# Kernel optimization log

Measured on AMD Instinct MI355X. Metric: run time of the kernel, lower is better.

The kernel has to match this reference:

```python
import math
import jax, jax.numpy as jnp
import numpy as np

N_LAYERS = 6
N_HEADS = 8
WINDOW = 4
LN_EPS = 1e-6


def _get_rel_emb(emb, length):
    # emb: [1, 2*WINDOW+1, kc] -> [1, 2*length-1, kc]
    max_rel = 2 * WINDOW + 1
    pad = max(0, length - (WINDOW + 1))
    start = max(0, WINDOW + 1 - length)
    end = max_rel + 2 * length - 1
    if pad > 0:
        emb = jnp.pad(emb, ((0, 0), (pad, pad), (0, 0)))
    return emb[:, start:end]


def _rel_to_abs(x):
    # x: [b,h,l,2l-1] -> [b,h,l,l]
    b, h, l, _ = x.shape
    x = jnp.pad(x, ((0, 0), (0, 0), (0, 0), (0, 1)))
    xf = x.reshape(b, h, l * 2 * l)
    xf = jnp.pad(xf, ((0, 0), (0, 0), (0, l - 1)))
    return xf.reshape(b, h, l + 1, 2 * l - 1)[:, :, :l, l - 1:]


def _abs_to_rel(x):
    # x: [b,h,l,l] -> [b,h,l,2l-1]
    b, h, l, _ = x.shape
    x = jnp.pad(x, ((0, 0), (0, 0), (0, 0), (0, l - 1)))
    xf = x.reshape(b, h, -1)
    xf = jnp.pad(xf, ((0, 0), (0, 0), (l, 0)))
    return xf.reshape(b, h, l, 2 * l)[..., 1:]


def _layer_norm(x, scale, bias):
    m = jnp.mean(x, axis=-1, keepdims=True)
    v = jnp.mean(jnp.square(x - m), axis=-1, keepdims=True)
    return (x - m) * jax.lax.rsqrt(v + LN_EPS) * scale + bias


def _forward(x, x_mask, Wq, bq, Wk, bk, Wv, bv, Wo, bo, emb_rel_k, emb_rel_v,
             ln1_scale, ln1_bias, W1, b1, W2, b2, ln2_scale, ln2_bias):
    B, T, C = x.shape
    H = N_HEADS
    KC = C // H
    scale = 1.0 / math.sqrt(KC)
    attn_mask = x_mask[:, :, None, :] * x_mask[:, :, :, None]  # [B,1,T,T]
    mask_t = jnp.transpose(x_mask, (0, 2, 1))  # [B,T,1]
    x = x * mask_t
    for l in range(N_LAYERS):
        # --- relative-position multi-head self-attention ---
        q = (x @ Wq[l] + bq[l]).reshape(B, T, H, KC).transpose(0, 2, 1, 3)
        k = (x @ Wk[l] + bk[l]).reshape(B, T, H, KC).transpose(0, 2, 1, 3)
        v = (x @ Wv[l] + bv[l]).reshape(B, T, H, KC).transpose(0, 2, 1, 3)
        scores = jnp.einsum('bhqd,bhkd->bhqk', q * scale, k)
        rk = _get_rel_emb(emb_rel_k[l], T)[0]  # [2T-1, KC] (heads shared)
        rel_logits = jnp.einsum('bhld,md->bhlm', q * scale, rk)
        scores = scores + _rel_to_abs(rel_logits)
        scores = jnp.where(attn_mask == 0, -10000.0, scores)
        p = jax.nn.softmax(scores, axis=-1)
        out = jnp.einsum('bhqk,bhkd->bhqd', p, v)
        rv = _get_rel_emb(emb_rel_v[l], T)[0]
        out = out + jnp.einsum('bhlm,md->bhld', _abs_to_rel(p), rv)
        out = out.transpose(0, 2, 1, 3).reshape(B, T, C)
        y = out @ Wo[l] + bo[l]
        x = _layer_norm(x + y, ln1_scale[l], ln1_bias[l])
        # --- pointwise conv FFN (kernel_size=1) ---
        h1 = jax.nn.relu((x * mask_t) @ W1[l] + b1[l])
        y = (h1 * mask_t) @ W2[l] + b2[l]
        y = y * mask_t
        x = _layer_norm(x + y, ln2_scale[l], ln2_bias[l])
    return x * mask_t


def setup_inputs() -> dict:
    key = jax.random.key(0)
    B, T, C, F, L, H = 8, 768, 512, 2048, N_LAYERS, N_HEADS
    KC = C // H
    ks = jax.random.split(key, 10)
    nrm = lambda k, s, sd=0.02: jax.random.normal(k, s, jnp.float32) * sd
    return {
        'x': jax.random.normal(ks[0], (B, T, C), jnp.float32),
        'x_mask': jnp.ones((B, 1, T), jnp.float32),
        'Wq': nrm(ks[1], (L, C, C)), 'bq': jnp.zeros((L, C), jnp.float32),
        'Wk': nrm(ks[2], (L, C, C)), 'bk': jnp.zeros((L, C), jnp.float32),
        'Wv': nrm(ks[3], (L, C, C)), 'bv': jnp.zeros((L, C), jnp.float32),
        'Wo': nrm(ks[4], (L, C, C)), 'bo': jnp.zeros((L, C), jnp.float32),
        'emb_rel_k': nrm(ks[5], (L, 1, 2 * WINDOW + 1, KC), KC ** -0.5),
        'emb_rel_v': nrm(ks[6], (L, 1, 2 * WINDOW + 1, KC), KC ** -0.5),
        'ln1_scale': jnp.ones((L, C), jnp.float32), 'ln1_bias': jnp.zeros((L, C), jnp.float32),
        'W1': nrm(ks[7], (L, C, F)), 'b1': jnp.zeros((L, F), jnp.float32),
        'W2': nrm(ks[8], (L, F, C)), 'b2': jnp.zeros((L, C), jnp.float32),
        'ln2_scale': jnp.ones((L, C), jnp.float32), 'ln2_bias': jnp.zeros((L, C), jnp.float32),
    }


def reference(x, x_mask, Wq, bq, Wk, bk, Wv, bv, Wo, bo, emb_rel_k, emb_rel_v,
              ln1_scale, ln1_bias, W1, b1, W2, b2, ln2_scale, ln2_bias):
    return _forward(x, x_mask, Wq, bq, Wk, bk, Wv, bv, Wo, bo, emb_rel_k, emb_rel_v,
                    ln1_scale, ln1_bias, W1, b1, W2, b2, ln2_scale, ln2_bias)
```

## Files before the change

### kernel.cpp

```cpp
#include <hip/hip_runtime.h>
#include <stdint.h>


typedef unsigned short u16;
typedef __attribute__((ext_vector_type(8))) __bf16 bf16x8;
typedef __attribute__((ext_vector_type(4))) float f32x4;

#define B_ 8
#define T_ 768
#define C_ 512
#define F_ 2048
#define LOG2E 1.4426950408889634f

__device__ __forceinline__ float b2f(u16 u) {
    union { float f; uint32_t i; } x; x.i = ((uint32_t)u) << 16; return x.f;
}
__device__ __forceinline__ u16 f2b(float f) {
    union { float f; uint32_t i; } x; x.f = f;
    return (u16)((x.i + 0x7fffu + ((x.i >> 16) & 1u)) >> 16);
}

template <int EPI>
__global__ __launch_bounds__(256) void gemm_bt4(
    const u16* __restrict__ A, int aStride,
    const u16* __restrict__ Bt, int bStride,
    const float* __restrict__ bias,
    u16* __restrict__ out, int oStride, int K, float epiScale)
{
    const int tid = threadIdx.x;
    const int wave = tid >> 6, lane = tid & 63;
    const int wm = wave & 1, wn = wave >> 1;
    const int quad = lane >> 4, l16 = lane & 15;
    const int m0 = blockIdx.x * 64;
    const int n0 = blockIdx.y * 64;

    __shared__ u16 As[64 * 64];
    __shared__ u16 Bs[64 * 64];

    const f32x4 vzero = {0.f, 0.f, 0.f, 0.f};
    f32x4 acc[2][2];
#pragma unroll
    for (int i = 0; i < 2; ++i)
#pragma unroll
        for (int j = 0; j < 2; ++j) acc[i][j] = vzero;

    for (int k0 = 0; k0 < K; k0 += 64) {
#pragma unroll
        for (int i = 0; i < 2; ++i) {
            int c = tid + i * 256;
            int row = c >> 3, pc = c & 7, lc = pc ^ (row & 7);
            *(uint4*)&As[c * 8] =
                *(const uint4*)(A + (long long)(m0 + row) * aStride + (k0 + lc * 8));
            *(uint4*)&Bs[c * 8] =
                *(const uint4*)(Bt + (long long)(n0 + row) * bStride + (k0 + lc * 8));
        }
        __syncthreads();
        __builtin_amdgcn_s_setprio(1);
#pragma unroll
        for (int ks = 0; ks < 2; ++ks) {
            bf16x8 af[2], bfr[2];
#pragma unroll
            for (int mi = 0; mi < 2; ++mi) {
                int row = wm * 32 + mi * 16 + l16;
                int pc = ((ks << 2) | quad) ^ (row & 7);
                af[mi] = *(const bf16x8*)&As[row * 64 + pc * 8];
            }
#pragma unroll
            for (int ni = 0; ni < 2; ++ni) {
                int row = wn * 32 + ni * 16 + l16;
                int pc = ((ks << 2) | quad) ^ (row & 7);
                bfr[ni] = *(const bf16x8*)&Bs[row * 64 + pc * 8];
            }
#pragma unroll
            for (int mi = 0; mi < 2; ++mi)
#pragma unroll
                for (int ni = 0; ni < 2; ++ni)
                    acc[mi][ni] = __builtin_amdgcn_mfma_f32_16x16x32_bf16(
                        bfr[ni], af[mi], acc[mi][ni], 0, 0, 0);
        }
        __builtin_amdgcn_s_setprio(0);
        __syncthreads();
    }

#pragma unroll
    for (int mi = 0; mi < 2; ++mi) {
        int row = m0 + wm * 32 + mi * 16 + l16;
#pragma unroll
        for (int ni = 0; ni < 2; ++ni) {
            int colb = n0 + wn * 32 + ni * 16 + quad * 4;
            u16 pk[4];
#pragma unroll
            for (int r = 0; r < 4; ++r) {
                float v = acc[mi][ni][r] + bias[colb + r];
                if (EPI == 1) v = v > 0.f ? v : 0.f;
                if (EPI == 3) { if (colb + r < 512) v *= epiScale; }
                pk[r] = f2b(v);
            }
            uint2 p;
            p.x = (uint32_t)pk[0] | ((uint32_t)pk[1] << 16);
            p.y = (uint32_t)pk[2] | ((uint32_t)pk[3] << 16);
            *(uint2*)(out + (long long)row * oStride + colb) = p;
        }
    }
}

__global__ __launch_bounds__(256) void bandg_k(
    const u16* __restrict__ qkv, const float* __restrict__ erk,
    float* __restrict__ bandg)
{
    __shared__ float erkS[576];
    const int tid = threadIdx.x;
    for (int idx = tid; idx < 576; idx += 256) erkS[idx] = erk[idx];
    __syncthreads();
    const int gid = blockIdx.x * 256 + tid;
    const int row = gid >> 3, h = gid & 7;
    const u16* q = qkv + (long long)row * 1536 + h * 64;
    float acc[9];
#pragma unroll
    for (int e = 0; e < 9; ++e) acc[e] = 0.f;
#pragma unroll
    for (int c = 0; c < 8; ++c) {
        uint4 d4 = *(const uint4*)(q + c * 8);
        const uint32_t dw[4] = {d4.x, d4.y, d4.z, d4.w};
#pragma unroll
        for (int j = 0; j < 8; ++j) {
            u16 uu = (u16)((dw[j >> 1] >> ((j & 1) * 16)) & 0xffff);
            float qv = b2f(uu);
            int d = c * 8 + j;
#pragma unroll
            for (int e = 0; e < 9; ++e) acc[e] += qv * erkS[e * 64 + d];
        }
    }
    float* o = bandg + (long long)gid * 9;
#pragma unroll
    for (int e = 0; e < 9; ++e) o[e] = acc[e];
}

__global__ __launch_bounds__(256) void flash_attn(
    const u16* __restrict__ qkv, const u16* __restrict__ vt,
    const float* __restrict__ mask, const float* __restrict__ bandg,
    const float* __restrict__ erv, u16* __restrict__ outb)
{
    const int tid = threadIdx.x;
    const int w = tid >> 6, lane = tid & 63;
    const int quad = lane >> 4, l16 = lane & 15;
    const int orig = blockIdx.y * 12 + blockIdx.x;
    const int swz = (orig & 7) * 96 + (orig >> 3);
    const int qt = swz % 12, bh = swz / 12;
    const int b = bh >> 3, h = bh & 7;
    const int q0 = qt * 64;

    __shared__ u16 Ql[64 * 64];
    __shared__ u16 Kt[2][64 * 64];
    __shared__ u16 Vt[2][64 * 64];
    __shared__ u16 Pl[4][16 * 64];
    __shared__ float bandk[64][10];
    __shared__ float maskK[2][64];

#pragma unroll
    for (int i = 0; i < 2; ++i) {
        int c = tid + i * 256;
        int r = c >> 3, pc = c & 7, lc = pc ^ (r & 7);
        *(uint4*)&Ql[c * 8] =
            *(const uint4*)(qkv + (long long)(b * T_ + q0 + r) * 1536 + h * 64 + lc * 8);
    }
#pragma unroll
    for (int i = 0; i < 2; ++i) {
        int c = tid + i * 256;
        int r = c >> 3, pc = c & 7, lc = pc ^ (r & 7);
        *(uint4*)&Kt[0][c * 8] =
            *(const uint4*)(qkv + (long long)(b * T_ + r) * 1536 + 512 + h * 64 + lc * 8);
        *(uint4*)&Vt[0][c * 8] =
            *(const uint4*)(vt + ((long long)bh * 64 + r) * T_ + lc * 8);
    }
    if (tid < 64) maskK[0][tid] = mask[b * T_ + tid];
    for (int idx = tid; idx < 576; idx += 256) {
        int r = idx / 9, e = idx - r * 9;
        bandk[r][e] = bandg[((long long)(b * T_ + q0 + r) * 8 + h) * 9 + e];
    }

    const int i_row = q0 + w * 16 + l16;
    const float mi = mask[b * T_ + i_row];
    float m_run = -1e30f, l_run = 0.f;
    const f32x4 vzero = {0.f, 0.f, 0.f, 0.f};
    f32x4 vacc[4] = {vzero, vzero, vzero, vzero};
    float pb[3] = {0.f, 0.f, 0.f};

    __syncthreads();
    bf16x8 qf[2];
#pragma unroll
    for (int ks = 0; ks < 2; ++ks) {
        int r = w * 16 + l16;
        int pc = ((ks << 2) | quad) ^ (r & 7);
        qf[ks] = *(const bf16x8*)&Ql[r * 64 + pc * 8];
    }

    int cbuf = 0;
    for (int kt = 0; kt < 12; ++kt) {
        uint4 kreg[2], vreg[2];
        float mreg = 0.f;
        const bool pre = (kt < 11);
        if (pre) {
            const int ktn = kt + 1;
#pragma unroll
            for (int i = 0; i < 2; ++i) {
                int c = tid + i * 256;
                int r = c >> 3, pc = c & 7, lc = pc ^ (r & 7);
                kreg[i] = *(const uint4*)(qkv + (long long)(b * T_ + ktn * 64 + r) * 1536
                                          + 512 + h * 64 + lc * 8);
                vreg[i] = *(const uint4*)(vt + ((long long)bh * 64 + r) * T_
                                          + ktn * 64 + lc * 8);
            }
            if (tid < 64) mreg = mask[b * T_ + ktn * 64 + tid];
        }

        const float mkv = maskK[cbuf][lane];
        const bool tile_clean = (__ballot(mkv == 0.f) == 0ull);
        const bool fast = tile_clean && (mi != 0.f);
        const bool has_band = (kt * 64 <= q0 + w * 16 + 19) &&
                              (kt * 64 + 67 >= q0 + w * 16);

        f32x4 sacc[4];
#pragma unroll
        for (int ni = 0; ni < 4; ++ni) sacc[ni] = vzero;
        __builtin_amdgcn_s_setprio(1);
#pragma unroll
        for (int ks = 0; ks < 2; ++ks)
#pragma unroll
            for (int ni = 0; ni < 4; ++ni) {
                int r = ni * 16 + l16;
                int pc = ((ks << 2) | quad) ^ (r & 7);
                bf16x8 kf = *(const bf16x8*)&Kt[cbuf][r * 64 + pc * 8];
                sacc[ni] = __builtin_amdgcn_mfma_f32_16x16x32_bf16(kf, qf[ks], sacc[ni], 0, 0, 0);
            }
        __builtin_amdgcn_s_setprio(0);

        if (has_band) {
#pragma unroll
            for (int ni = 0; ni < 4; ++ni)
#pragma unroll
                for (int r = 0; r < 4; ++r) {
                    int jl = ni * 16 + quad * 4 + r;
                    int dlt = kt * 64 + jl - i_row;
                    if (dlt >= -4 && dlt <= 4)
                        sacc[ni][r] += bandk[w * 16 + l16][dlt + 4];
                }
        }
        if (!fast) {
#pragma unroll
            for (int ni = 0; ni < 4; ++ni)
#pragma unroll
                for (int r = 0; r < 4; ++r) {
                    int jl = ni * 16 + quad * 4 + r;
                    if (mi * maskK[cbuf][jl] == 0.f) sacc[ni][r] = -14427.0f;
                }
        }

        float mx;
        {
            float a0 = fmaxf(sacc[0][0], sacc[0][1]), a1 = fmaxf(sacc[0][2], sacc[0][3]);
            float b0 = fmaxf(sacc[1][0], sacc[1][1]), b1 = fmaxf(sacc[1][2], sacc[1][3]);
            float c0 = fmaxf(sacc[2][0], sacc[2][1]), c1 = fmaxf(sacc[2][2], sacc[2][3]);
            float d0 = fmaxf(sacc[3][0], sacc[3][1]), d1 = fmaxf(sacc[3][2], sacc[3][3]);
            float t0 = fmaxf(fmaxf(a0, a1), fmaxf(b0, b1));
            float t1 = fmaxf(fmaxf(c0, c1), fmaxf(d0, d1));
            mx = fmaxf(t0, t1);
        }
        mx = fmaxf(mx, __shfl_xor(mx, 16));
        mx = fmaxf(mx, __shfl_xor(mx, 32));
        float m_new = fmaxf(m_run, mx);
        if (__any(mx > m_run)) {
            float alpha = exp2f(m_run - m_new);
            l_run *= alpha;
#pragma unroll
            for (int ni = 0; ni < 4; ++ni) vacc[ni] = vacc[ni] * alpha;
#pragma unroll
            for (int k = 0; k < 3; ++k) pb[k] *= alpha;
        }
        m_run = m_new;

        float lsum = 0.f;
#pragma unroll
        for (int ni = 0; ni < 4; ++ni) {
            float u0 = exp2f(sacc[ni][0] - m_new);
            float u1 = exp2f(sacc[ni][1] - m_new);
            float u2 = exp2f(sacc[ni][2] - m_new);
            float u3 = exp2f(sacc[ni][3] - m_new);
            lsum += (u0 + u1) + (u2 + u3);
            union { __bf16 h[2]; uint32_t u; } cA, cB;
            cA.h[0] = (__bf16)u0; cA.h[1] = (__bf16)u1;
            cB.h[0] = (__bf16)u2; cB.h[1] = (__bf16)u3;
            int c0 = ni * 16 + quad * 4;
            int phys = (((c0 >> 3) ^ (l16 & 7)) << 3) + (c0 & 7);
            uint2 p; p.x = cA.u; p.y = cB.u;
            *(uint2*)&Pl[w][l16 * 64 + phys] = p;
        }
        l_run += lsum;

        if (has_band) {
#pragma unroll
            for (int k = 0; k < 3; ++k) {
                int e = quad * 3 + k;
                if (e < 9) {
                    int jl = i_row + e - 4 - kt * 64;
                    if (jl >= 0 && jl < 64) {
                        int phys = (((jl >> 3) ^ (l16 & 7)) << 3) + (jl & 7);
                        pb[k] += b2f(Pl[w][l16 * 64 + phys]);
                    }
                }
            }
        }

        __builtin_amdgcn_s_setprio(1);
#pragma unroll
        for (int ks = 0; ks < 2; ++ks) {
            int pcc = ((ks << 2) | quad) ^ (l16 & 7);
            bf16x8 pf = *(const bf16x8*)&Pl[w][l16 * 64 + pcc * 8];
#pragma unroll
            for (int ni = 0; ni < 4; ++ni) {
                int r = ni * 16 + l16;
                int pc = ((ks << 2) | quad) ^ (r & 7);
                bf16x8 vf = *(const bf16x8*)&Vt[cbuf][r * 64 + pc * 8];
                vacc[ni] = __builtin_amdgcn_mfma_f32_16x16x32_bf16(vf, pf, vacc[ni], 0, 0, 0);
            }
        }
        __builtin_amdgcn_s_setprio(0);

        if (pre) {
#pragma unroll
            for (int i = 0; i < 2; ++i) {
                int c = tid + i * 256;
                *(uint4*)&Kt[cbuf ^ 1][c * 8] = kreg[i];
                *(uint4*)&Vt[cbuf ^ 1][c * 8] = vreg[i];
            }
            if (tid < 64) maskK[cbuf ^ 1][tid] = mreg;
            __syncthreads();
            cbuf ^= 1;
        }
    }

    l_run += __shfl_xor(l_run, 16);
    l_run += __shfl_xor(l_run, 32);
    const float rinv = 1.f / l_run;

    float pband[9];
#pragma unroll
    for (int e = 0; e < 9; ++e) {
        float val = (quad == e / 3) ? pb[e % 3] : 0.f;
        val += __shfl_xor(val, 16);
        val += __shfl_xor(val, 32);
        pband[e] = val * rinv;
    }

    u16* orow = outb + (long long)(b * T_ + i_row) * C_ + h * 64;
#pragma unroll
    for (int ni = 0; ni < 4; ++ni) {
        u16 pk[4];
#pragma unroll
        for (int r = 0; r < 4; ++r) {
            int d = ni * 16 + quad * 4 + r;
            float v = vacc[ni][r] * rinv;
#pragma unroll
            for (int e = 0; e < 9; ++e) v += pband[e] * erv[e * 64 + d];
            pk[r] = f2b(v);
        }
        uint2 p;
        p.x = (uint32_t)pk[0] | ((uint32_t)pk[1] << 16);
        p.y = (uint32_t)pk[2] | ((uint32_t)pk[3] << 16);
        *(uint2*)(orow + ni * 16 + quad * 4) = p;
    }
}

__global__ void transpose_qkvo(const float* __restrict__ Wq, const float* __restrict__ Wk,
                               const float* __restrict__ Wv, const float* __restrict__ Wo,
                               u16* __restrict__ wqkvT, u16* __restrict__ woT)
{
    __shared__ u16 tile[32][33];
    const int z = blockIdx.z, l = z >> 2, which = z & 3;
    const float* src = (which == 0 ? Wq : which == 1 ? Wk : which == 2 ? Wv : Wo)
                       + (long long)l * 262144;
    u16* dst = (which == 3) ? woT + (long long)l * 262144
                            : wqkvT + (long long)l * 786432 + which * 262144;
    const int r0 = blockIdx.y * 32, c0 = blockIdx.x * 32;
    const int tx = threadIdx.x, ty = threadIdx.y;
#pragma unroll
    for (int i = 0; i < 32; i += 8)
        tile[ty + i][tx] = f2b(src[(long long)(r0 + ty + i) * 512 + (c0 + tx)]);
    __syncthreads();
#pragma unroll
    for (int i = 0; i < 32; i += 8)
        dst[(long long)(c0 + ty + i) * 512 + (r0 + tx)] = tile[tx][ty + i];
}

__global__ void transpose_f2bL(const float* __restrict__ src0, int sStride, long long sLayer,
                               u16* __restrict__ dst0, int dStride, long long dLayer)
{
    __shared__ u16 tile[32][33];
    const int l = blockIdx.z;
    const float* src = src0 + (long long)l * sLayer;
    u16* dst = dst0 + (long long)l * dLayer;
    const int r0 = blockIdx.y * 32, c0 = blockIdx.x * 32;
    const int tx = threadIdx.x, ty = threadIdx.y;
#pragma unroll
    for (int i = 0; i < 32; i += 8)
        tile[ty + i][tx] = f2b(src[(long long)(r0 + ty + i) * sStride + (c0 + tx)]);
    __syncthreads();
#pragma unroll
    for (int i = 0; i < 32; i += 8)
        dst[(long long)(c0 + ty + i) * dStride + (r0 + tx)] = tile[tx][ty + i];
}

__global__ void transpose_b(const u16* __restrict__ src, long long sB1, long long sB2, int sStride,
                            u16* __restrict__ dst, long long dB1, long long dB2, int dStride)
{
    __shared__ u16 tile[32][33];
    const int z = blockIdx.z, zb = z >> 3, zh = z & 7;
    src += (long long)zb * sB1 + (long long)zh * sB2;
    dst += (long long)zb * dB1 + (long long)zh * dB2;
    const int r0 = blockIdx.y * 32, c0 = blockIdx.x * 32;
    const int tx = threadIdx.x, ty = threadIdx.y;
#pragma unroll
    for (int i = 0; i < 32; i += 8)
        tile[ty + i][tx] = src[(long long)(r0 + ty + i) * sStride + (c0 + tx)];
    __syncthreads();
#pragma unroll
    for (int i = 0; i < 32; i += 8)
        dst[(long long)(c0 + ty + i) * dStride + (r0 + tx)] = tile[tx][ty + i];
}

__global__ void concat_bias(const float* __restrict__ bq, const float* __restrict__ bk,
                            const float* __restrict__ bv, float* __restrict__ dst)
{
    int i = blockIdx.x * 256 + threadIdx.x;
    int l = i / 1536, n = i - l * 1536;
    float v = (n < 512) ? bq[l * 512 + n]
             : (n < 1024 ? bk[l * 512 + (n - 512)] : bv[l * 512 + (n - 1024)]);
    dst[i] = v;
}

__global__ void mask_in(const float* __restrict__ x, const float* __restrict__ mask,
                        u16* __restrict__ out)
{
    int i4 = (blockIdx.x * 256 + threadIdx.x) * 4;
    float4 xv = *(const float4*)(x + i4);
    float m = mask[i4 >> 9];
    u16 pk[4] = {f2b(xv.x * m), f2b(xv.y * m), f2b(xv.z * m), f2b(xv.w * m)};
    uint2 p; p.x = (uint32_t)pk[0] | ((uint32_t)pk[1] << 16);
    p.y = (uint32_t)pk[2] | ((uint32_t)pk[3] << 16);
    *(uint2*)(out + i4) = p;
}

__global__ void mask_out(const u16* __restrict__ x, const float* __restrict__ mask,
                         float* __restrict__ out)
{
    int i4 = (blockIdx.x * 256 + threadIdx.x) * 4;
    uint2 p = *(const uint2*)(x + i4);
    float m = mask[i4 >> 9];
    float4 o;
    o.x = b2f((u16)(p.x & 0xffff)) * m;
    o.y = b2f((u16)(p.x >> 16)) * m;
    o.z = b2f((u16)(p.y & 0xffff)) * m;
    o.w = b2f((u16)(p.y >> 16)) * m;
    *(float4*)(out + i4) = o;
}

__global__ __launch_bounds__(256) void add_ln(
    const u16* __restrict__ x, const u16* __restrict__ y,
    const float* __restrict__ sc, const float* __restrict__ bi,
    u16* __restrict__ outx)
{
    const int wave = threadIdx.x >> 6, lane = threadIdx.x & 63;
    const long long r = (long long)blockIdx.x * 4 + wave;
    const u16* xr = x + r * C_;
    const u16* yr = y + r * C_;
    float v[8], s = 0.f;
#pragma unroll
    for (int it = 0; it < 2; ++it) {
        int j0 = it * 256 + lane * 4;
        uint2 px = *(const uint2*)(xr + j0);
        uint2 py = *(const uint2*)(yr + j0);
        v[it * 4 + 0] = b2f((u16)(px.x & 0xffff)) + b2f((u16)(py.x & 0xffff));
        v[it * 4 + 1] = b2f((u16)(px.x >> 16))    + b2f((u16)(py.x >> 16));
        v[it * 4 + 2] = b2f((u16)(px.y & 0xffff)) + b2f((u16)(py.y & 0xffff));
        v[it * 4 + 3] = b2f((u16)(px.y >> 16))    + b2f((u16)(py.y >> 16));
        s += v[it * 4 + 0] + v[it * 4 + 1] + v[it * 4 + 2] + v[it * 4 + 3];
    }
#pragma unroll
    for (int off = 32; off > 0; off >>= 1) s += __shfl_down(s, off);
    s = __shfl(s, 0);
    const float mean = s * (1.f / 512.f);
    float var = 0.f;
#pragma unroll
    for (int l = 0; l < 8; ++l) { float d = v[l] - mean; var += d * d; }
#pragma unroll
    for (int off = 32; off > 0; off >>= 1) var += __shfl_down(var, off);
    var = __shfl(var, 0);
    const float rs = rsqrtf(var * (1.f / 512.f) + 1e-6f);
    u16* orow = outx + r * C_;
#pragma unroll
    for (int it = 0; it < 2; ++it) {
        int j0 = it * 256 + lane * 4;
        float4 s4 = *(const float4*)(sc + j0);
        float4 b4 = *(const float4*)(bi + j0);
        u16 pk[4];
        pk[0] = f2b((v[it * 4 + 0] - mean) * rs * s4.x + b4.x);
        pk[1] = f2b((v[it * 4 + 1] - mean) * rs * s4.y + b4.y);
        pk[2] = f2b((v[it * 4 + 2] - mean) * rs * s4.z + b4.z);
        pk[3] = f2b((v[it * 4 + 3] - mean) * rs * s4.w + b4.w);
        uint2 p; p.x = (uint32_t)pk[0] | ((uint32_t)pk[1] << 16);
        p.y = (uint32_t)pk[2] | ((uint32_t)pk[3] << 16);
        *(uint2*)(orow + j0) = p;
    }
}

extern "C" void kernel_launch(void* const* d_in, const int* in_sizes, int n_in,
                              void* d_out, int out_size, void* d_ws, size_t ws_size,
                              hipStream_t stream)
{
    const float* x    = (const float*)d_in[0];
    const float* mask = (const float*)d_in[1];
    const float* Wq   = (const float*)d_in[2];
    const float* bq   = (const float*)d_in[3];
    const float* Wk   = (const float*)d_in[4];
    const float* bk   = (const float*)d_in[5];
    const float* Wv   = (const float*)d_in[6];
    const float* bv   = (const float*)d_in[7];
    const float* Wo   = (const float*)d_in[8];
    const float* bo   = (const float*)d_in[9];
    const float* erk  = (const float*)d_in[10];
    const float* erv  = (const float*)d_in[11];
    const float* ln1s = (const float*)d_in[12];
    const float* ln1b = (const float*)d_in[13];
    const float* W1   = (const float*)d_in[14];
    const float* b1   = (const float*)d_in[15];
    const float* W2   = (const float*)d_in[16];
    const float* b2   = (const float*)d_in[17];
    const float* ln2s = (const float*)d_in[18];
    const float* ln2b = (const float*)d_in[19];
    float* out = (float*)d_out;
    u16* ws  = (u16*)d_ws;

    const long long CF = 512LL * 2048;
    const int M = B_ * T_;

    u16* wqkvT   = ws;
    u16* woT     = ws + 4718592;
    u16* w1T     = ws + 6291456;
    u16* w2T     = ws + 12582912;
    float* bqkv  = (float*)(ws + 18874368);
    u16* xb      = ws + 18892800;
    u16* qkvb    = ws + 22038528;
    u16* vtb     = ws + 31475712;
    u16* attnb   = ws + 34621440;
    u16* scr     = ws + 37767168;
    float* bandg = (float*)(ws + 50350080);
    u16* yb      = vtb;

    const dim3 tb(32, 8);

    transpose_qkvo<<<dim3(16, 16, 24), tb, 0, stream>>>(Wq, Wk, Wv, Wo, wqkvT, woT);
    transpose_f2bL<<<dim3(64, 16, 6), tb, 0, stream>>>(W1, 2048, CF, w1T, 512, 1048576);
    transpose_f2bL<<<dim3(16, 64, 6), tb, 0, stream>>>(W2, 512,  CF, w2T, 2048, 1048576);
    concat_bias<<<36, 256, 0, stream>>>(bq, bk, bv, bqkv);
    mask_in<<<(M * 512) / 1024, 256, 0, stream>>>(x, mask, xb);

    for (int l = 0; l < 6; ++l) {
        gemm_bt4<3><<<dim3(96, 24), 256, 0, stream>>>(
            xb, 512, wqkvT + (long long)l * 786432, 512, bqkv + l * 1536,
            qkvb, 1536, 512, 0.125f * LOG2E);
        bandg_k<<<192, 256, 0, stream>>>(qkvb, erk + l * 576, bandg);
        transpose_b<<<dim3(2, 24, 64), tb, 0, stream>>>(
            qkvb + 1024, 768LL * 1536, 64, 1536,
            vtb, 8LL * 64 * 768, 64LL * 768, 768);
        flash_attn<<<dim3(12, 64), 256, 0, stream>>>(
            qkvb, vtb, mask, bandg, erv + l * 576, attnb);
        gemm_bt4<0><<<dim3(96, 8), 256, 0, stream>>>(
            attnb, 512, woT + (long long)l * 262144, 512, bo + l * 512,
            yb, 512, 512, 0.f);
        add_ln<<<1536, 256, 0, stream>>>(xb, yb, ln1s + l * 512, ln1b + l * 512, xb);
        gemm_bt4<1><<<dim3(96, 32), 256, 0, stream>>>(
            xb, 512, w1T + (long long)l * 1048576, 512, b1 + l * 2048,
            scr, 2048, 512, 0.f);
        gemm_bt4<0><<<dim3(96, 8), 256, 0, stream>>>(
            scr, 2048, w2T + (long long)l * 1048576, 2048, b2 + l * 512,
            yb, 512, 2048, 0.f);
        add_ln<<<1536, 256, 0, stream>>>(xb, yb, ln2s + l * 512, ln2b + l * 512, xb);
    }

    mask_out<<<(M * 512) / 1024, 256, 0, stream>>>(xb, mask, out);
}
```

Baseline: 1.067 ms.

## Shrink flash attention blocks to 32 queries and drop K/V double-buffering

Flash attention now runs 128-thread blocks that each cover 32 query rows, giving twice as many blocks. The register-prefetched double buffer for K/V tiles is replaced by a single shared buffer loaded synchronously between two barriers each iteration. The online-softmax rescale now runs unconditionally instead of behind an __any check. The aim is to cut LDS and register use so more blocks fit per CU, but it gives up load/compute overlap and makes each block re-read K/V for fewer queries, which doubles global K/V traffic.

Measured after the change: 1.017 ms. 1.05x faster.

```diff
diff --git a/kernel.cpp b/kernel.cpp
--- a/kernel.cpp
+++ b/kernel.cpp
@@ -136,7 +136,7 @@
     for (int e = 0; e < 9; ++e) o[e] = acc[e];
 }
 
-__global__ __launch_bounds__(256) void flash_attn(
+__global__ __launch_bounds__(128) void flash_attn(
     const u16* __restrict__ qkv, const u16* __restrict__ vt,
     const float* __restrict__ mask, const float* __restrict__ bandg,
     const float* __restrict__ erv, u16* __restrict__ outb)
@@ -144,37 +144,27 @@
     const int tid = threadIdx.x;
     const int w = tid >> 6, lane = tid & 63;
     const int quad = lane >> 4, l16 = lane & 15;
-    const int orig = blockIdx.y * 12 + blockIdx.x;
-    const int swz = (orig & 7) * 96 + (orig >> 3);
-    const int qt = swz % 12, bh = swz / 12;
+    const int orig = blockIdx.y * 24 + blockIdx.x;
+    const int swz = (orig & 7) * 192 + (orig >> 3);
+    const int qt = swz % 24, bh = swz / 24;
     const int b = bh >> 3, h = bh & 7;
-    const int q0 = qt * 64;
-
-    __shared__ u16 Ql[64 * 64];
-    __shared__ u16 Kt[2][64 * 64];
-    __shared__ u16 Vt[2][64 * 64];
-    __shared__ u16 Pl[4][16 * 64];
-    __shared__ float bandk[64][10];
-    __shared__ float maskK[2][64];
+    const int q0 = qt * 32;
+
+    __shared__ u16 Ql[32 * 64];
+    __shared__ u16 Kt[64 * 64];
+    __shared__ u16 Vt[64 * 64];
+    __shared__ u16 Pl[2][16 * 64];
+    __shared__ float bandk[32][10];
+    __shared__ float maskK[64];
 
 #pragma unroll
     for (int i = 0; i < 2; ++i) {
-        int c = tid + i * 256;
+        int c = tid + i * 128;
         int r = c >> 3, pc = c & 7, lc = pc ^ (r & 7);
         *(uint4*)&Ql[c * 8] =
             *(const uint4*)(qkv + (long long)(b * T_ + q0 + r) * 1536 + h * 64 + lc * 8);
     }
-#pragma unroll
-    for (int i = 0; i < 2; ++i) {
-        int c = tid + i * 256;
-        int r = c >> 3, pc = c & 7, lc = pc ^ (r & 7);
-        *(uint4*)&Kt[0][c * 8] =
-            *(const uint4*)(qkv + (long long)(b * T_ + r) * 1536 + 512 + h * 64 + lc * 8);
-        *(uint4*)&Vt[0][c * 8] =
-            *(const uint4*)(vt + ((long long)bh * 64 + r) * T_ + lc * 8);
-    }
-    if (tid < 64) maskK[0][tid] = mask[b * T_ + tid];
-    for (int idx = tid; idx < 576; idx += 256) {
+    for (int idx = tid; idx < 288; idx += 128) {
         int r = idx / 9, e = idx - r * 9;
         bandk[r][e] = bandg[((long long)(b * T_ + q0 + r) * 8 + h) * 9 + e];
     }
@@ -195,26 +185,21 @@
         qf[ks] = *(const bf16x8*)&Ql[r * 64 + pc * 8];
     }
 
-    int cbuf = 0;
     for (int kt = 0; kt < 12; ++kt) {
-        uint4 kreg[2], vreg[2];
-        float mreg = 0.f;
-        const bool pre = (kt < 11);
-        if (pre) {
-            const int ktn = kt + 1;
-#pragma unroll
-            for (int i = 0; i < 2; ++i) {
-                int c = tid + i * 256;
-                int r = c >> 3, pc = c & 7, lc = pc ^ (r & 7);
-                kreg[i] = *(const uint4*)(qkv + (long long)(b * T_ + ktn * 64 + r) * 1536
-                                          + 512 + h * 64 + lc * 8);
-                vreg[i] = *(const uint4*)(vt + ((long long)bh * 64 + r) * T_
-                                          + ktn * 64 + lc * 8);
-            }
-            if (tid < 64) mreg = mask[b * T_ + ktn * 64 + tid];
-        }
-
-        const float mkv = maskK[cbuf][lane];
+        __syncthreads();
+#pragma unroll
+        for (int i = 0; i < 4; ++i) {
+            int c = tid + i * 128;
+            int r = c >> 3, pc = c & 7, lc = pc ^ (r & 7);
+            *(uint4*)&Kt[c * 8] =
+                *(const uint4*)(qkv + (long long)(b * T_ + kt * 64 + r) * 1536 + 512 + h * 64 + lc * 8);
+            *(uint4*)&Vt[c * 8] =
+                *(const uint4*)(vt + ((long long)bh * 64 + r) * T_ + kt * 64 + lc * 8);
+        }
+        if (tid < 64) maskK[tid] = mask[b * T_ + kt * 64 + tid];
+        __syncthreads();
+
+        const float mkv = maskK[lane];
         const bool tile_clean = (__ballot(mkv == 0.f) == 0ull);
         const bool fast = tile_clean && (mi != 0.f);
         const bool has_band = (kt * 64 <= q0 + w * 16 + 19) &&
@@ -230,7 +215,7 @@
             for (int ni = 0; ni < 4; ++ni) {
                 int r = ni * 16 + l16;
                 int pc = ((ks << 2) | quad) ^ (r & 7);
-                bf16x8 kf = *(const bf16x8*)&Kt[cbuf][r * 64 + pc * 8];
+                bf16x8 kf = *(const bf16x8*)&Kt[r * 64 + pc * 8];
                 sacc[ni] = __builtin_amdgcn_mfma_f32_16x16x32_bf16(kf, qf[ks], sacc[ni], 0, 0, 0);
             }
         __builtin_amdgcn_s_setprio(0);
@@ -252,7 +237,7 @@
 #pragma unroll
                 for (int r = 0; r < 4; ++r) {
                     int jl = ni * 16 + quad * 4 + r;
-                    if (mi * maskK[cbuf][jl] == 0.f) sacc[ni][r] = -14427.0f;
+                    if (mi * maskK[jl] == 0.f) sacc[ni][r] = -14427.0f;
                 }
         }
 
@@ -268,16 +253,14 @@
         }
         mx = fmaxf(mx, __shfl_xor(mx, 16));
         mx = fmaxf(mx, __shfl_xor(mx, 32));
-        float m_new = fmaxf(m_run, mx);
-        if (__any(mx > m_run)) {
-            float alpha = exp2f(m_run - m_new);
-            l_run *= alpha;
-#pragma unroll
-            for (int ni = 0; ni < 4; ++ni) vacc[ni] = vacc[ni] * alpha;
-#pragma unroll
-            for (int k = 0; k < 3; ++k) pb[k] *= alpha;
-        }
+        const float m_new = fmaxf(m_run, mx);
+        const float alpha = exp2f(m_run - m_new);
         m_run = m_new;
+        l_run *= alpha;
+#pragma unroll
+        for (int ni = 0; ni < 4; ++ni) vacc[ni] = vacc[ni] * alpha;
+#pragma unroll
+        for (int k = 0; k < 3; ++k) pb[k] *= alpha;
 
         float lsum = 0.f;
 #pragma unroll
@@ -320,23 +303,11 @@
             for (int ni = 0; ni < 4; ++ni) {
                 int r = ni * 16 + l16;
                 int pc = ((ks << 2) | quad) ^ (r & 7);
-                bf16x8 vf = *(const bf16x8*)&Vt[cbuf][r * 64 + pc * 8];
+                bf16x8 vf = *(const bf16x8*)&Vt[r * 64 + pc * 8];
                 vacc[ni] = __builtin_amdgcn_mfma_f32_16x16x32_bf16(vf, pf, vacc[ni], 0, 0, 0);
             }
         }
         __builtin_amdgcn_s_setprio(0);
-
-        if (pre) {
-#pragma unroll
-            for (int i = 0; i < 2; ++i) {
-                int c = tid + i * 256;
-                *(uint4*)&Kt[cbuf ^ 1][c * 8] = kreg[i];
-                *(uint4*)&Vt[cbuf ^ 1][c * 8] = vreg[i];
-            }
-            if (tid < 64) maskK[cbuf ^ 1][tid] = mreg;
-            __syncthreads();
-            cbuf ^= 1;
-        }
     }
 
     l_run += __shfl_xor(l_run, 16);
@@ -572,7 +543,7 @@
         transpose_b<<<dim3(2, 24, 64), tb, 0, stream>>>(
             qkvb + 1024, 768LL * 1536, 64, 1536,
             vtb, 8LL * 64 * 768, 64LL * 768, 768);
-        flash_attn<<<dim3(12, 64), 256, 0, stream>>>(
+        flash_attn<<<dim3(24, 64), 128, 0, stream>>>(
             qkvb, vtb, mask, bandg, erv + l * 576, attnb);
         gemm_bt4<0><<<dim3(96, 8), 256, 0, stream>>>(
             attnb, 512, woT + (long long)l * 262144, 512, bo + l * 512,
```
